# Performance work log

Measured on AMD Instinct MI355X. Metric: run time of the kernel, lower is better.

## Reference

```python
import jax, jax.numpy as jnp
import numpy as np
import math

N, L, C, H = 16, 2048, 512, 8
D = C // H  # head channels = 64


def setup_inputs() -> dict:
    key = jax.random.key(0)
    ks = jax.random.split(key, 18)
    s = 1.0 / math.sqrt(C)
    sd = 1.0 / math.sqrt(D)
    return {
        "x_q": jax.random.normal(ks[0], (N, L, C), jnp.float32),
        "x_kv": jax.random.normal(ks[1], (N, L, C), jnp.float32),
        "Wq": jax.random.normal(ks[2], (C, C), jnp.float32) * s,
        "bq": jax.random.normal(ks[3], (C,), jnp.float32) * s,
        "wqa": jax.random.normal(ks[4], (D,), jnp.float32) * sd,
        "bqa": jax.random.normal(ks[5], (1,), jnp.float32) * sd,
        "Wk": jax.random.normal(ks[6], (C, C), jnp.float32) * s,
        "bk": jax.random.normal(ks[7], (C,), jnp.float32) * s,
        "wka": jax.random.normal(ks[8], (D,), jnp.float32) * sd,
        "bka": jax.random.normal(ks[9], (1,), jnp.float32) * sd,
        "Wv": jax.random.normal(ks[10], (C, C), jnp.float32) * s,
        "bv": jax.random.normal(ks[11], (C,), jnp.float32) * s,
        "Wt": jax.random.normal(ks[12], (D, D), jnp.float32) * sd,
        "bt": jax.random.normal(ks[13], (D,), jnp.float32) * sd,
        "Wp": jax.random.normal(ks[14], (C, C), jnp.float32) * s,
        "bp": jax.random.normal(ks[15], (C,), jnp.float32) * s,
    }


def _separate_heads(x):
    # (N, L, C) -> (N, H, L, D)
    n, l, _ = x.shape
    return x.reshape(n, l, H, D).transpose(0, 2, 1, 3)


def reference(x_q, x_kv, Wq, bq, wqa, bqa, Wk, bk, wka, bka, Wv, bv, Wt, bt, Wp, bp):
    inv_sqrt_d = 1.0 / math.sqrt(D)

    # Query projection (torch Linear: y = x @ W.T + b), dropout is identity (eval)
    q = _separate_heads(x_q @ Wq.T + bq)  # (N,H,L,D)
    # Additive pooling of queries over L
    q_score = (jnp.einsum("nhld,d->nhl", q, wqa) + bqa[0]) * inv_sqrt_d
    q_weight = jax.nn.softmax(q_score, axis=-1)  # (N,H,L)
    pooled_q = jnp.einsum("nhl,nhld->nhd", q_weight, q)[:, :, None, :]  # (N,H,1,D)

    # Key projection, gated by pooled query
    k = _separate_heads(x_kv @ Wk.T + bk)  # (N,H,L,D)
    kq = k * pooled_q
    k_score = (jnp.einsum("nhld,d->nhl", kq, wka) + bka[0]) * inv_sqrt_d
    k_weight = jax.nn.softmax(k_score, axis=-1)
    pooled_k = jnp.einsum("nhl,nhld->nhd", k_weight, k)[:, :, None, :]  # (N,H,1,D)

    # Value projection, gated by pooled key, then per-head transform
    v = _separate_heads(x_kv @ Wv.T + bv)  # (N,H,L,D)
    kv = jnp.einsum("nhld,ed->nhle", v * pooled_k, Wt) + bt

    out = kv + q  # (N,H,L,D)
    out = out.transpose(0, 2, 1, 3).reshape(out.shape[0], out.shape[2], C)  # group heads
    return out @ Wp.T + bp
```

## Files before the change

kernel.cpp:

```cpp
#include <hip/hip_runtime.h>
#include <hip/hip_bf16.h>
#include <math.h>

#define NB 16
#define LL 2048
#define CC 512
#define HH 8
#define MM (NB*LL)

typedef __attribute__((ext_vector_type(8))) short bf16x8;
typedef __attribute__((ext_vector_type(4))) float f32x4;
typedef __attribute__((ext_vector_type(8))) unsigned short u16x8;

__device__ inline unsigned short f2bf(float x) {
    __hip_bfloat16 b = __float2bfloat16(x);
    return __builtin_bit_cast(unsigned short, b);
}
__device__ inline float bf2f(unsigned short u) {
    __hip_bfloat16 b = __builtin_bit_cast(__hip_bfloat16, u);
    return __bfloat162float(b);
}
__device__ inline void split2(float x, unsigned short& h, unsigned short& l) {
    unsigned short hh = f2bf(x);
    float fh = bf2f(hh);
    h = hh;
    l = f2bf(x - fh);
}

__global__ __launch_bounds__(256)
void prep_kernel(const float* __restrict__ Wq, const float* __restrict__ Wk,
                 const float* __restrict__ Wv, const float* __restrict__ Wt,
                 const float* __restrict__ bt, const float* __restrict__ Wp,
                 const float* __restrict__ bp,
                 unsigned short* __restrict__ Bqh, unsigned short* __restrict__ Bql,
                 unsigned short* __restrict__ Bkh, unsigned short* __restrict__ Bkl,
                 unsigned short* __restrict__ Bvh, unsigned short* __restrict__ Bvl,
                 unsigned short* __restrict__ WPTh, unsigned short* __restrict__ WPTl,
                 float* __restrict__ WBFP, float* __restrict__ cvec)
{
    const int t = blockIdx.x * 256 + threadIdx.x;
    const int c = t >> 10;
    const int k = t & 1023;
    unsigned short hh, ll;
    if (k < 512) {
        const int h = k >> 6, d = k & 63;
        float s = 0.f;
        #pragma unroll 8
        for (int e = 0; e < 64; ++e) s += Wt[e * 64 + d] * Wp[c * CC + h * 64 + e];
        const size_t pq = (((size_t)(k >> 3) * 512) + c) * 8 + (k & 7);
        WBFP[pq] = s;
        split2(Wq[c * CC + k], hh, ll); Bqh[pq] = hh; Bql[pq] = ll;
        split2(Wk[c * CC + k], hh, ll); Bkh[pq] = hh; Bkl[pq] = ll;
        split2(Wv[c * CC + k], hh, ll); Bvh[pq] = hh; Bvl[pq] = ll;
    } else {
        const int kl = k - 512;
        const size_t pw = (((size_t)(kl >> 3) * 512) + c) * 8 + (kl & 7);
        split2(Wp[c * CC + kl], hh, ll);
        WPTh[pw] = hh; WPTl[pw] = ll;
    }
    if (k == 0) {
        float cv = bp[c];
        for (int j = 0; j < 512; ++j) cv += bt[j & 63] * Wp[c * CC + j];
        cvec[c] = cv;
    }
}

__global__ __launch_bounds__(256)
void gate_wb(const float* __restrict__ WBFP, const float* __restrict__ pk,
             unsigned short* __restrict__ WBGh, unsigned short* __restrict__ WBGl)
{
    const int u = blockIdx.x * 256 + threadIdx.x;
    const int smp = u >> 15;
    const int r = u & 32767;
    const int kp = r >> 9, c = r & 511;
    const float* w = &WBFP[(((size_t)kp * 512) + c) * 8];
    const float* p = &pk[smp * 512 + kp * 8];
    u16x8 hv, lv;
    #pragma unroll
    for (int j = 0; j < 8; ++j) {
        unsigned short h, lo;
        split2(w[j] * p[j], h, lo);
        hv[j] = h; lv[j] = lo;
    }
    const size_t o = (((size_t)smp * 64 + kp) * 512 + c) * 8;
    *(u16x8*)&WBGh[o] = hv;
    *(u16x8*)&WBGl[o] = lv;
}

__global__ __launch_bounds__(512, 4)
void gemm_proj(const float* __restrict__ A0, const float* __restrict__ A1,
               const unsigned short* __restrict__ B0h, const unsigned short* __restrict__ B0l,
               const unsigned short* __restrict__ B1h, const unsigned short* __restrict__ B1l,
               const float* __restrict__ bias0, const float* __restrict__ bias1,
               unsigned short* __restrict__ O0h, unsigned short* __restrict__ O0l,
               unsigned short* __restrict__ O1h, unsigned short* __restrict__ O1l,
               int ntl)
{
    __shared__ __align__(16) unsigned short smem[24576];
    unsigned short* sAh = smem;
    unsigned short* sAl = smem + 4096;
    unsigned short* sBh = smem + 8192;
    unsigned short* sBl = smem + 16384;

    const int tid = threadIdx.x;
    const int flat = blockIdx.x;
    const int xcd = flat & 7, idx = flat >> 3;
    const int mt = xcd * 32 + (idx >> ntl);
    const int ntv = idx & ((1 << ntl) - 1);
    const int type = ntv >> 1;
    const int n0 = (ntv & 1) * 256;
    const int m0 = mt * 128;
    const int l = tid & 63, w = tid >> 6;
    const int wm = w >> 2, wn = w & 3;

    const float* Asrc = type ? A1 : A0;
    const unsigned short* Bh = type ? B1h : B0h;
    const unsigned short* Bl = type ? B1l : B0l;
    const float* bias = type ? bias1 : bias0;
    unsigned short* Oh = type ? O1h : O0h;
    unsigned short* Ol = type ? O1l : O0l;

    const int arow = tid & 127, akp = tid >> 7;
    const int bcol = tid & 255, bkp0 = tid >> 8;

    f32x4 acc[4][4] = {};

    float4 pa0, pa1;
    uint4 pbh0, pbh1, pbl0, pbl1;

    auto loadTile = [&](int kt) {
        const int k0 = kt * 32;
        const float* p = Asrc + (size_t)(m0 + arow) * CC + k0 + akp * 8;
        pa0 = *(const float4*)p; pa1 = *(const float4*)(p + 4);
        const int kpg = kt * 4;
        const size_t ob0 = (((size_t)(kpg + bkp0) * 512) + n0 + bcol) * 8;
        const size_t ob1 = (((size_t)(kpg + bkp0 + 2) * 512) + n0 + bcol) * 8;
        pbh0 = *(const uint4*)&Bh[ob0]; pbh1 = *(const uint4*)&Bh[ob1];
        pbl0 = *(const uint4*)&Bl[ob0]; pbl1 = *(const uint4*)&Bl[ob1];
    };

    auto storeTile = [&]() {
        float x[8];
        *(float4*)&x[0] = pa0; *(float4*)&x[4] = pa1;
        u16x8 hv, lv;
        #pragma unroll
        for (int j = 0; j < 8; ++j) { unsigned short h, lo; split2(x[j], h, lo); hv[j] = h; lv[j] = lo; }
        *(u16x8*)&sAh[(akp * 128 + arow) * 8] = hv;
        *(u16x8*)&sAl[(akp * 128 + arow) * 8] = lv;
        *(uint4*)&sBh[(bkp0 * 256 + bcol) * 8] = pbh0;
        *(uint4*)&sBh[((bkp0 + 2) * 256 + bcol) * 8] = pbh1;
        *(uint4*)&sBl[(bkp0 * 256 + bcol) * 8] = pbl0;
        *(uint4*)&sBl[((bkp0 + 2) * 256 + bcol) * 8] = pbl1;
    };

    loadTile(0);

    for (int kt = 0; kt < 16; ++kt) {
        __syncthreads();
        storeTile();
        __syncthreads();
        if (kt + 1 < 16) loadTile(kt + 1);

        const int g = l >> 4;
        const int rA = wm * 64 + (l & 15);
        const int rB = wn * 64 + (l & 15);
        const bf16x8* vAh = (const bf16x8*)sAh; const bf16x8* vAl = (const bf16x8*)sAl;
        const bf16x8* vBh = (const bf16x8*)sBh; const bf16x8* vBl = (const bf16x8*)sBl;
        bf16x8 ah[4], al[4], bh[4], bl[4];
        #pragma unroll
        for (int f = 0; f < 4; ++f) {
            ah[f] = vAh[g * 128 + rA + f * 16];
            al[f] = vAl[g * 128 + rA + f * 16];
            bh[f] = vBh[g * 256 + rB + f * 16];
            bl[f] = vBl[g * 256 + rB + f * 16];
        }
        #pragma unroll
        for (int i = 0; i < 4; ++i)
            #pragma unroll
            for (int j = 0; j < 4; ++j) {
                acc[i][j] = __builtin_amdgcn_mfma_f32_16x16x32_bf16(ah[i], bh[j], acc[i][j], 0, 0, 0);
                acc[i][j] = __builtin_amdgcn_mfma_f32_16x16x32_bf16(ah[i], bl[j], acc[i][j], 0, 0, 0);
                acc[i][j] = __builtin_amdgcn_mfma_f32_16x16x32_bf16(al[i], bh[j], acc[i][j], 0, 0, 0);
            }
    }

    const int rowb = (l >> 4) * 4, colb = l & 15;
    const int hw = wn >> 1;
    const int clbase = (wn & 1) * 64;
    unsigned short* sP = smem;
    for (int half = 0; half < 2; ++half) {
        for (int part = 0; part < 2; ++part) {
            __syncthreads();
            if (hw == half) {
                #pragma unroll
                for (int j = 0; j < 4; ++j) {
                    const float bv = bias[n0 + half * 128 + clbase + j * 16 + colb];
                    #pragma unroll
                    for (int i = 0; i < 4; ++i) {
                        #pragma unroll
                        for (int e = 0; e < 4; ++e) {
                            const int row = wm * 64 + i * 16 + rowb + e;
                            const int cl = clbase + j * 16 + colb;
                            unsigned short h, lo;
                            split2(acc[i][j][e] + bv, h, lo);
                            sP[row * 132 + cl] = part ? lo : h;
                        }
                    }
                }
            }
            __syncthreads();
            unsigned short* OP = part ? Ol : Oh;
            #pragma unroll
            for (int pass = 0; pass < 4; ++pass) {
                const int o = pass * 4 + (tid >> 7);
                const int row = tid & 127;
                const uint2 v0 = *(const uint2*)&sP[row * 132 + o * 8];
                const uint2 v1 = *(const uint2*)&sP[row * 132 + o * 8 + 4];
                const int cg = n0 + half * 128 + o * 8;
                uint4 val; val.x = v0.x; val.y = v0.y; val.z = v1.x; val.w = v1.y;
                *(uint4*)&OP[((size_t)(cg >> 3) * MM + m0 + row) * 8] = val;
            }
        }
    }
}

__global__ __launch_bounds__(512, 4)
void gemm_final(const unsigned short* __restrict__ VPh, const unsigned short* __restrict__ VPl,
                const unsigned short* __restrict__ QPh, const unsigned short* __restrict__ QPl,
                const unsigned short* __restrict__ WBGh, const unsigned short* __restrict__ WBGl,
                const unsigned short* __restrict__ WPTh, const unsigned short* __restrict__ WPTl,
                const float* __restrict__ cvec, float* __restrict__ out)
{
    __shared__ __align__(16) unsigned short smem[24576];
    unsigned short* sAh = smem;
    unsigned short* sAl = smem + 4096;
    unsigned short* sBh = smem + 8192;
    unsigned short* sBl = smem + 16384;

    const int tid = threadIdx.x;
    const int flat = blockIdx.x;
    const int xcd = flat & 7, idx = flat >> 3;
    const int mt = xcd * 32 + (idx >> 1);
    const int nt = idx & 1;
    const int n0 = nt * 256, m0 = mt * 128;
    const int l = tid & 63, w = tid >> 6;
    const int wm = w >> 2, wn = w & 3;
    const int smp = mt >> 4;

    const int arow = tid & 127, akp = tid >> 7;
    const int bcol = tid & 255, bkp0 = tid >> 8;

    f32x4 acc[4][4] = {};

    uint4 pah, pal, pbh0, pbh1, pbl0, pbl1;

    auto loadTile = [&](int kt) {
        const int ktl = kt & 15;
        const unsigned short* Ah_ = (kt < 16) ? VPh : QPh;
        const unsigned short* Al_ = (kt < 16) ? VPl : QPl;
        const size_t ao = (((size_t)ktl * 4 + akp) * MM + m0 + arow) * 8;
        pah = *(const uint4*)&Ah_[ao];
        pal = *(const uint4*)&Al_[ao];
        const unsigned short* Bh_;
        const unsigned short* Bl_;
        size_t bb;
        if (kt < 16) { Bh_ = WBGh + (size_t)smp * 262144; Bl_ = WBGl + (size_t)smp * 262144; bb = kt * 4; }
        else         { Bh_ = WPTh; Bl_ = WPTl; bb = (kt - 16) * 4; }
        const size_t ob0 = ((bb + bkp0) * 512 + n0 + bcol) * 8;
        const size_t ob1 = ((bb + bkp0 + 2) * 512 + n0 + bcol) * 8;
        pbh0 = *(const uint4*)&Bh_[ob0]; pbh1 = *(const uint4*)&Bh_[ob1];
        pbl0 = *(const uint4*)&Bl_[ob0]; pbl1 = *(const uint4*)&Bl_[ob1];
    };

    auto storeTile = [&]() {
        *(uint4*)&sAh[(akp * 128 + arow) * 8] = pah;
        *(uint4*)&sAl[(akp * 128 + arow) * 8] = pal;
        *(uint4*)&sBh[(bkp0 * 256 + bcol) * 8] = pbh0;
        *(uint4*)&sBh[((bkp0 + 2) * 256 + bcol) * 8] = pbh1;
        *(uint4*)&sBl[(bkp0 * 256 + bcol) * 8] = pbl0;
        *(uint4*)&sBl[((bkp0 + 2) * 256 + bcol) * 8] = pbl1;
    };

    loadTile(0);

    for (int kt = 0; kt < 32; ++kt) {
        __syncthreads();
        storeTile();
        __syncthreads();
        if (kt + 1 < 32) loadTile(kt + 1);

        const int g = l >> 4;
        const int rA = wm * 64 + (l & 15);
        const int rB = wn * 64 + (l & 15);
        const bf16x8* vAh = (const bf16x8*)sAh; const bf16x8* vAl = (const bf16x8*)sAl;
        const bf16x8* vBh = (const bf16x8*)sBh; const bf16x8* vBl = (const bf16x8*)sBl;
        bf16x8 ah[4], al[4], bh[4], bl[4];
        #pragma unroll
        for (int f = 0; f < 4; ++f) {
            ah[f] = vAh[g * 128 + rA + f * 16];
            al[f] = vAl[g * 128 + rA + f * 16];
            bh[f] = vBh[g * 256 + rB + f * 16];
            bl[f] = vBl[g * 256 + rB + f * 16];
        }
        #pragma unroll
        for (int i = 0; i < 4; ++i)
            #pragma unroll
            for (int j = 0; j < 4; ++j) {
                acc[i][j] = __builtin_amdgcn_mfma_f32_16x16x32_bf16(ah[i], bh[j], acc[i][j], 0, 0, 0);
                acc[i][j] = __builtin_amdgcn_mfma_f32_16x16x32_bf16(ah[i], bl[j], acc[i][j], 0, 0, 0);
                acc[i][j] = __builtin_amdgcn_mfma_f32_16x16x32_bf16(al[i], bh[j], acc[i][j], 0, 0, 0);
            }
    }

    const int rowb = (l >> 4) * 4, colb = l & 15;
    #pragma unroll
    for (int j = 0; j < 4; ++j) {
        const int c = n0 + wn * 64 + j * 16 + colb;
        const float bv = cvec[c];
        #pragma unroll
        for (int i = 0; i < 4; ++i) {
            const int r = m0 + wm * 64 + i * 16 + rowb;
            #pragma unroll
            for (int e = 0; e < 4; ++e)
                out[(size_t)(r + e) * CC + c] = acc[i][j][e] + bv;
        }
    }
}

__global__ __launch_bounds__(256)
void pool_stage1(const unsigned short* __restrict__ Ph, const unsigned short* __restrict__ Pl,
                 const float* __restrict__ wvec, const float* __restrict__ bscal,
                 float* __restrict__ partials, int modeK)
{
    __shared__ float sm[256];
    __shared__ float se[4];
    const int nh = blockIdx.x, chunk = blockIdx.y;
    const int n = nh >> 3, h = nh & 7;
    const int tid = threadIdx.x;
    const int wave = tid >> 6, d = tid & 63;
    const float wv = modeK ? wvec[nh * 64 + d] : wvec[d];
    const float b = bscal[0];
    const size_t rbase = ((size_t)(h * 8 + (d >> 3))) * MM + (size_t)n * LL;
    const int kc = d & 7;
    float accv = 0.f, acce = 0.f;
    const int l0 = chunk * 128 + wave;
    #pragma unroll 4
    for (int it = 0; it < 32; ++it) {
        const int ll = l0 + it * 4;
        const size_t a = (rbase + ll) * 8 + kc;
        const float x = bf2f(Ph[a]) + bf2f(Pl[a]);
        float s = x * wv;
        s += __shfl_xor(s, 1, 64);
        s += __shfl_xor(s, 2, 64);
        s += __shfl_xor(s, 4, 64);
        s += __shfl_xor(s, 8, 64);
        s += __shfl_xor(s, 16, 64);
        s += __shfl_xor(s, 32, 64);
        const float e = expf((s + b) * 0.125f);
        accv += e * x;
        acce += e;
    }
    sm[tid] = accv;
    if (d == 0) se[wave] = acce;
    __syncthreads();
    if (wave == 0) {
        const float pv = sm[d] + sm[64 + d] + sm[128 + d] + sm[192 + d];
        float* pr = partials + ((size_t)nh * 16 + chunk) * 65;
        pr[d] = pv;
        if (d == 0) pr[64] = se[0] + se[1] + se[2] + se[3];
    }
}

__global__ __launch_bounds__(64)
void pool_stage2(const float* __restrict__ partials, const float* __restrict__ postmul,
                 float* __restrict__ pooled)
{
    const int nh = blockIdx.x, d = threadIdx.x;
    float pv = 0.f, pe = 0.f;
    #pragma unroll
    for (int c = 0; c < 16; ++c) {
        const float* pr = partials + ((size_t)nh * 16 + c) * 65;
        pv += pr[d];
        pe += pr[64];
    }
    float p = pv / pe;
    if (postmul) p *= postmul[d];
    pooled[nh * 64 + d] = p;
}

#define OFF_BQH   0ull
#define OFF_BQL   524288ull
#define OFF_BKH   1048576ull
#define OFF_BKL   1572864ull
#define OFF_BVH   2097152ull
#define OFF_BVL   2621440ull
#define OFF_WPTH  3145728ull
#define OFF_WPTL  3670016ull
#define OFF_WBFP  4194304ull
#define OFF_CVEC  5242880ull
#define OFF_GQ    5246976ull
#define OFF_PK    5279744ull
#define OFF_PART  5312512ull
#define OFF_WBGH  6291456ull
#define OFF_WBGL  14680064ull
#define OFF_QPH   23068672ull
#define OFF_QPL   56623104ull
#define OFF_KPH   90177536ull
#define OFF_KPL   123731968ull

extern "C" void kernel_launch(void* const* d_in, const int* in_sizes, int n_in,
                              void* d_out, int out_size, void* d_ws, size_t ws_size,
                              hipStream_t stream) {
    const float* x_q  = (const float*)d_in[0];
    const float* x_kv = (const float*)d_in[1];
    const float* Wq   = (const float*)d_in[2];
    const float* bq   = (const float*)d_in[3];
    const float* wqa  = (const float*)d_in[4];
    const float* bqa  = (const float*)d_in[5];
    const float* Wk   = (const float*)d_in[6];
    const float* bk   = (const float*)d_in[7];
    const float* wka  = (const float*)d_in[8];
    const float* bka  = (const float*)d_in[9];
    const float* Wv   = (const float*)d_in[10];
    const float* bv   = (const float*)d_in[11];
    const float* Wt   = (const float*)d_in[12];
    const float* bt   = (const float*)d_in[13];
    const float* Wp   = (const float*)d_in[14];
    const float* bp   = (const float*)d_in[15];
    float* out = (float*)d_out;
    char* ws = (char*)d_ws;

    unsigned short* Bqh  = (unsigned short*)(ws + OFF_BQH);
    unsigned short* Bql  = (unsigned short*)(ws + OFF_BQL);
    unsigned short* Bkh  = (unsigned short*)(ws + OFF_BKH);
    unsigned short* Bkl  = (unsigned short*)(ws + OFF_BKL);
    unsigned short* Bvh  = (unsigned short*)(ws + OFF_BVH);
    unsigned short* Bvl  = (unsigned short*)(ws + OFF_BVL);
    unsigned short* WPTh = (unsigned short*)(ws + OFF_WPTH);
    unsigned short* WPTl = (unsigned short*)(ws + OFF_WPTL);
    float* WBFP = (float*)(ws + OFF_WBFP);
    float* cvec = (float*)(ws + OFF_CVEC);
    float* gq   = (float*)(ws + OFF_GQ);
    float* pk   = (float*)(ws + OFF_PK);
    float* part = (float*)(ws + OFF_PART);
    unsigned short* WBGh = (unsigned short*)(ws + OFF_WBGH);
    unsigned short* WBGl = (unsigned short*)(ws + OFF_WBGL);
    unsigned short* QPh  = (unsigned short*)(ws + OFF_QPH);
    unsigned short* QPl  = (unsigned short*)(ws + OFF_QPL);
    unsigned short* KPh  = (unsigned short*)(ws + OFF_KPH);
    unsigned short* KPl  = (unsigned short*)(ws + OFF_KPL);

    const dim3 pgrid(NB * HH, 16);

    prep_kernel<<<2048, 256, 0, stream>>>(Wq, Wk, Wv, Wt, bt, Wp, bp,
                                          Bqh, Bql, Bkh, Bkl, Bvh, Bvl,
                                          WPTh, WPTl, WBFP, cvec);
    gemm_proj<<<1024, 512, 0, stream>>>(x_q, x_kv, Bqh, Bql, Bkh, Bkl, bq, bk,
                                        QPh, QPl, KPh, KPl, 2);
    pool_stage1<<<pgrid, 256, 0, stream>>>(QPh, QPl, wqa, bqa, part, 0);
    pool_stage2<<<NB * HH, 64, 0, stream>>>(part, wka, gq);
    pool_stage1<<<pgrid, 256, 0, stream>>>(KPh, KPl, gq, bka, part, 1);
    pool_stage2<<<NB * HH, 64, 0, stream>>>(part, nullptr, pk);
    gate_wb<<<2048, 256, 0, stream>>>(WBFP, pk, WBGh, WBGl);
    gemm_proj<<<512, 512, 0, stream>>>(x_kv, x_kv, Bvh, Bvl, Bvh, Bvl, bv, bv,
                                       KPh, KPl, KPh, KPl, 1);
    gemm_final<<<512, 512, 0, stream>>>(KPh, KPl, QPh, QPl, WBGh, WBGl,
                                        WPTh, WPTl, cvec, out);
}
```

Baseline: 487.4 us.

## Pool queries and keys directly from inputs, skipping the full K projection

Folds the additive-pooling score vectors into the projection weights (Uq = Wq^T wqa, Uk = Wk^T gated wka), so the softmax scores and pooled sums are computed directly on raw x_q/x_kv. Pooled vectors are then projected once per batch item, which removes the full K projection GEMM and its bf16 hi/lo intermediate. The Q and V projections now share one GEMM launch. In exchange it adds a register-heavy pooling pass that reads x twice, a serial per-batch combine kernel, and a change in numerical rounding order.

```diff
diff --git a/kernel.cpp b/kernel.cpp
--- a/kernel.cpp
+++ b/kernel.cpp
@@ -28,12 +28,10 @@
 }
 
 __global__ __launch_bounds__(256)
-void prep_kernel(const float* __restrict__ Wq, const float* __restrict__ Wk,
-                 const float* __restrict__ Wv, const float* __restrict__ Wt,
-                 const float* __restrict__ bt, const float* __restrict__ Wp,
-                 const float* __restrict__ bp,
+void prep_kernel(const float* __restrict__ Wq, const float* __restrict__ Wv,
+                 const float* __restrict__ Wt, const float* __restrict__ bt,
+                 const float* __restrict__ Wp, const float* __restrict__ bp,
                  unsigned short* __restrict__ Bqh, unsigned short* __restrict__ Bql,
-                 unsigned short* __restrict__ Bkh, unsigned short* __restrict__ Bkl,
                  unsigned short* __restrict__ Bvh, unsigned short* __restrict__ Bvl,
                  unsigned short* __restrict__ WPTh, unsigned short* __restrict__ WPTl,
                  float* __restrict__ WBFP, float* __restrict__ cvec)
@@ -50,7 +48,6 @@
         const size_t pq = (((size_t)(k >> 3) * 512) + c) * 8 + (k & 7);
         WBFP[pq] = s;
         split2(Wq[c * CC + k], hh, ll); Bqh[pq] = hh; Bql[pq] = ll;
-        split2(Wk[c * CC + k], hh, ll); Bkh[pq] = hh; Bkl[pq] = ll;
         split2(Wv[c * CC + k], hh, ll); Bvh[pq] = hh; Bvl[pq] = ll;
     } else {
         const int kl = k - 512;
@@ -62,6 +59,153 @@
         float cv = bp[c];
         for (int j = 0; j < 512; ++j) cv += bt[j & 63] * Wp[c * CC + j];
         cvec[c] = cv;
+    }
+}
+
+__global__ __launch_bounds__(512)
+void uq_kernel(const float* __restrict__ Wq, const float* __restrict__ wqa,
+               const float* __restrict__ bqa, const float* __restrict__ bq,
+               float* __restrict__ Uq, float* __restrict__ qc)
+{
+    const int c = threadIdx.x;
+    float u[8] = {0.f,0.f,0.f,0.f,0.f,0.f,0.f,0.f};
+    for (int d = 0; d < 64; ++d) {
+        const float wv = wqa[d];
+        #pragma unroll
+        for (int h = 0; h < 8; ++h) u[h] += Wq[((size_t)(h * 64 + d)) * 512 + c] * wv;
+    }
+    #pragma unroll
+    for (int h = 0; h < 8; ++h) Uq[c * 8 + h] = u[h];
+    if (c < 8) {
+        float s = 0.f;
+        for (int d = 0; d < 64; ++d) s += bq[c * 64 + d] * wqa[d];
+        qc[c] = s + bqa[0];
+    }
+}
+
+__global__ __launch_bounds__(256)
+void pool_pass1(const float* __restrict__ x, const float* __restrict__ U, int ustride,
+                const float* __restrict__ cst, int cstride, float* __restrict__ part)
+{
+    __shared__ float ps2[2][8][512];
+    __shared__ float pe[4][8];
+    const int n = blockIdx.x, ch = blockIdx.y;
+    const int tid = threadIdx.x, wave = tid >> 6, lane = tid & 63;
+    const int c8 = lane * 8;
+    float u[64];
+    {
+        const float* Ub = U + (size_t)n * ustride + c8 * 8;
+        #pragma unroll
+        for (int j = 0; j < 16; ++j) *(float4*)&u[j * 4] = *(const float4*)&Ub[j * 4];
+    }
+    float cl[8];
+    #pragma unroll
+    for (int h = 0; h < 8; ++h) cl[h] = cst[n * cstride + h];
+    float acc[64];
+    #pragma unroll
+    for (int j = 0; j < 64; ++j) acc[j] = 0.f;
+    float ae[8] = {0.f,0.f,0.f,0.f,0.f,0.f,0.f,0.f};
+    const int l0 = ch * 64 + wave * 16;
+    const float* xb = x + ((size_t)n * LL + l0) * CC + c8;
+    for (int it = 0; it < 16; ++it) {
+        float xs[8];
+        *(float4*)&xs[0] = *(const float4*)&xb[(size_t)it * CC];
+        *(float4*)&xs[4] = *(const float4*)&xb[(size_t)it * CC + 4];
+        #pragma unroll
+        for (int h = 0; h < 8; ++h) {
+            float s = xs[0]*u[h]    + xs[1]*u[8+h]  + xs[2]*u[16+h] + xs[3]*u[24+h]
+                    + xs[4]*u[32+h] + xs[5]*u[40+h] + xs[6]*u[48+h] + xs[7]*u[56+h];
+            s += __shfl_xor(s, 1, 64);  s += __shfl_xor(s, 2, 64);
+            s += __shfl_xor(s, 4, 64);  s += __shfl_xor(s, 8, 64);
+            s += __shfl_xor(s, 16, 64); s += __shfl_xor(s, 32, 64);
+            const float e = __expf((s + cl[h]) * 0.125f);
+            ae[h] += e;
+            #pragma unroll
+            for (int j = 0; j < 8; ++j) acc[h * 8 + j] += e * xs[j];
+        }
+    }
+    if (wave < 2) {
+        #pragma unroll
+        for (int h = 0; h < 8; ++h)
+            #pragma unroll
+            for (int j = 0; j < 8; ++j) ps2[wave][h][c8 + j] = acc[h * 8 + j];
+    }
+    if (lane == 0) {
+        #pragma unroll
+        for (int h = 0; h < 8; ++h) pe[wave][h] = ae[h];
+    }
+    __syncthreads();
+    if (wave >= 2) {
+        #pragma unroll
+        for (int h = 0; h < 8; ++h)
+            #pragma unroll
+            for (int j = 0; j < 8; ++j) ps2[wave - 2][h][c8 + j] += acc[h * 8 + j];
+    }
+    __syncthreads();
+    float* pb = part + ((size_t)(n * 32 + ch)) * 4104;
+    for (int q = tid; q < 4096; q += 256) {
+        const int h = q >> 9, c = q & 511;
+        pb[q] = ps2[0][h][c] + ps2[1][h][c];
+    }
+    if (tid < 8) pb[4096 + tid] = pe[0][tid] + pe[1][tid] + pe[2][tid] + pe[3][tid];
+}
+
+__global__ __launch_bounds__(512)
+void pool_combine(const float* __restrict__ part,
+                  const float* __restrict__ W1, const float* __restrict__ b1,
+                  const float* __restrict__ wka,
+                  const float* __restrict__ Wk, const float* __restrict__ bk,
+                  const float* __restrict__ bka,
+                  float* __restrict__ gq, float* __restrict__ Uk,
+                  float* __restrict__ kc, float* __restrict__ pk, int mode)
+{
+    __shared__ float px[8][512];
+    __shared__ float inv[8];
+    __shared__ float gql[8][64];
+    const int n = blockIdx.x;
+    const int tid = threadIdx.x;
+    const float* pbase = part + (size_t)n * 32 * 4104;
+    for (int q = tid; q < 4096; q += 512) {
+        float s = 0.f;
+        for (int c2 = 0; c2 < 32; ++c2) s += pbase[(size_t)c2 * 4104 + q];
+        px[q >> 9][q & 511] = s;
+    }
+    if (tid < 8) {
+        float s = 0.f;
+        for (int c2 = 0; c2 < 32; ++c2) s += pbase[(size_t)c2 * 4104 + 4096 + tid];
+        inv[tid] = 1.f / s;
+    }
+    __syncthreads();
+    const int h = tid >> 6, d = tid & 63;
+    const int row = h * 64 + d;
+    float s = 0.f;
+    const float* wr = W1 + (size_t)row * 512;
+    #pragma unroll 8
+    for (int c = 0; c < 512; ++c) s += px[h][c] * wr[c];
+    const float pooled = s * inv[h] + b1[row];
+    if (mode == 0) {
+        const float g = pooled * wka[d];
+        gq[n * 512 + row] = g;
+        gql[h][d] = g;
+        __syncthreads();
+        const int c = tid & 511;
+        float uk[8];
+        #pragma unroll
+        for (int hh = 0; hh < 8; ++hh) uk[hh] = 0.f;
+        for (int dd = 0; dd < 64; ++dd) {
+            #pragma unroll
+            for (int hh = 0; hh < 8; ++hh)
+                uk[hh] += Wk[((size_t)(hh * 64 + dd)) * 512 + c] * gql[hh][dd];
+        }
+        #pragma unroll
+        for (int hh = 0; hh < 8; ++hh) Uk[(size_t)n * 4096 + c * 8 + hh] = uk[hh];
+        if (tid < 8) {
+            float kcv = 0.f;
+            for (int dd = 0; dd < 64; ++dd) kcv += bk[tid * 64 + dd] * gql[tid][dd];
+            kc[n * 8 + tid] = kcv + bka[0];
+        }
+    } else {
+        pk[n * 512 + row] = pooled;
     }
 }
 
@@ -327,86 +471,27 @@
     }
 }
 
-__global__ __launch_bounds__(256)
-void pool_stage1(const unsigned short* __restrict__ Ph, const unsigned short* __restrict__ Pl,
-                 const float* __restrict__ wvec, const float* __restrict__ bscal,
-                 float* __restrict__ partials, int modeK)
-{
-    __shared__ float sm[256];
-    __shared__ float se[4];
-    const int nh = blockIdx.x, chunk = blockIdx.y;
-    const int n = nh >> 3, h = nh & 7;
-    const int tid = threadIdx.x;
-    const int wave = tid >> 6, d = tid & 63;
-    const float wv = modeK ? wvec[nh * 64 + d] : wvec[d];
-    const float b = bscal[0];
-    const size_t rbase = ((size_t)(h * 8 + (d >> 3))) * MM + (size_t)n * LL;
-    const int kc = d & 7;
-    float accv = 0.f, acce = 0.f;
-    const int l0 = chunk * 128 + wave;
-    #pragma unroll 4
-    for (int it = 0; it < 32; ++it) {
-        const int ll = l0 + it * 4;
-        const size_t a = (rbase + ll) * 8 + kc;
-        const float x = bf2f(Ph[a]) + bf2f(Pl[a]);
-        float s = x * wv;
-        s += __shfl_xor(s, 1, 64);
-        s += __shfl_xor(s, 2, 64);
-        s += __shfl_xor(s, 4, 64);
-        s += __shfl_xor(s, 8, 64);
-        s += __shfl_xor(s, 16, 64);
-        s += __shfl_xor(s, 32, 64);
-        const float e = expf((s + b) * 0.125f);
-        accv += e * x;
-        acce += e;
-    }
-    sm[tid] = accv;
-    if (d == 0) se[wave] = acce;
-    __syncthreads();
-    if (wave == 0) {
-        const float pv = sm[d] + sm[64 + d] + sm[128 + d] + sm[192 + d];
-        float* pr = partials + ((size_t)nh * 16 + chunk) * 65;
-        pr[d] = pv;
-        if (d == 0) pr[64] = se[0] + se[1] + se[2] + se[3];
-    }
-}
-
-__global__ __launch_bounds__(64)
-void pool_stage2(const float* __restrict__ partials, const float* __restrict__ postmul,
-                 float* __restrict__ pooled)
-{
-    const int nh = blockIdx.x, d = threadIdx.x;
-    float pv = 0.f, pe = 0.f;
-    #pragma unroll
-    for (int c = 0; c < 16; ++c) {
-        const float* pr = partials + ((size_t)nh * 16 + c) * 65;
-        pv += pr[d];
-        pe += pr[64];
-    }
-    float p = pv / pe;
-    if (postmul) p *= postmul[d];
-    pooled[nh * 64 + d] = p;
-}
-
 #define OFF_BQH   0ull
 #define OFF_BQL   524288ull
-#define OFF_BKH   1048576ull
-#define OFF_BKL   1572864ull
-#define OFF_BVH   2097152ull
-#define OFF_BVL   2621440ull
-#define OFF_WPTH  3145728ull
-#define OFF_WPTL  3670016ull
-#define OFF_WBFP  4194304ull
-#define OFF_CVEC  5242880ull
-#define OFF_GQ    5246976ull
-#define OFF_PK    5279744ull
-#define OFF_PART  5312512ull
-#define OFF_WBGH  6291456ull
-#define OFF_WBGL  14680064ull
-#define OFF_QPH   23068672ull
-#define OFF_QPL   56623104ull
-#define OFF_KPH   90177536ull
-#define OFF_KPL   123731968ull
+#define OFF_BVH   1048576ull
+#define OFF_BVL   1572864ull
+#define OFF_WPTH  2097152ull
+#define OFF_WPTL  2621440ull
+#define OFF_WBFP  3145728ull
+#define OFF_CVEC  4194304ull
+#define OFF_UQ    4198400ull
+#define OFF_QC    4214784ull
+#define OFF_UK    4215040ull
+#define OFF_KC    4477184ull
+#define OFF_GQ    4477952ull
+#define OFF_PK    4510720ull
+#define OFF_PART  4543488ull
+#define OFF_WBGH  13107200ull
+#define OFF_WBGL  21495808ull
+#define OFF_QPH   29884416ull
+#define OFF_QPL   63438848ull
+#define OFF_VPH   96993280ull
+#define OFF_VPL   130547712ull
 
 extern "C" void kernel_launch(void* const* d_in, const int* in_sizes, int n_in,
                               void* d_out, int out_size, void* d_ws, size_t ws_size,
@@ -432,14 +517,16 @@
 
     unsigned short* Bqh  = (unsigned short*)(ws + OFF_BQH);
     unsigned short* Bql  = (unsigned short*)(ws + OFF_BQL);
-    unsigned short* Bkh  = (unsigned short*)(ws + OFF_BKH);
-    unsigned short* Bkl  = (unsigned short*)(ws + OFF_BKL);
     unsigned short* Bvh  = (unsigned short*)(ws + OFF_BVH);
     unsigned short* Bvl  = (unsigned short*)(ws + OFF_BVL);
     unsigned short* WPTh = (unsigned short*)(ws + OFF_WPTH);
     unsigned short* WPTl = (unsigned short*)(ws + OFF_WPTL);
     float* WBFP = (float*)(ws + OFF_WBFP);
     float* cvec = (float*)(ws + OFF_CVEC);
+    float* Uq   = (float*)(ws + OFF_UQ);
+    float* qc   = (float*)(ws + OFF_QC);
+    float* Uk   = (float*)(ws + OFF_UK);
+    float* kc   = (float*)(ws + OFF_KC);
     float* gq   = (float*)(ws + OFF_GQ);
     float* pk   = (float*)(ws + OFF_PK);
     float* part = (float*)(ws + OFF_PART);
@@ -447,23 +534,23 @@
     unsigned short* WBGl = (unsigned short*)(ws + OFF_WBGL);
     unsigned short* QPh  = (unsigned short*)(ws + OFF_QPH);
     unsigned short* QPl  = (unsigned short*)(ws + OFF_QPL);
-    unsigned short* KPh  = (unsigned short*)(ws + OFF_KPH);
-    unsigned short* KPl  = (unsigned short*)(ws + OFF_KPL);
-
-    const dim3 pgrid(NB * HH, 16);
-
-    prep_kernel<<<2048, 256, 0, stream>>>(Wq, Wk, Wv, Wt, bt, Wp, bp,
-                                          Bqh, Bql, Bkh, Bkl, Bvh, Bvl,
-                                          WPTh, WPTl, WBFP, cvec);
-    gemm_proj<<<1024, 512, 0, stream>>>(x_q, x_kv, Bqh, Bql, Bkh, Bkl, bq, bk,
-                                        QPh, QPl, KPh, KPl, 2);
-    pool_stage1<<<pgrid, 256, 0, stream>>>(QPh, QPl, wqa, bqa, part, 0);
-    pool_stage2<<<NB * HH, 64, 0, stream>>>(part, wka, gq);
-    pool_stage1<<<pgrid, 256, 0, stream>>>(KPh, KPl, gq, bka, part, 1);
-    pool_stage2<<<NB * HH, 64, 0, stream>>>(part, nullptr, pk);
+    unsigned short* VPh  = (unsigned short*)(ws + OFF_VPH);
+    unsigned short* VPl  = (unsigned short*)(ws + OFF_VPL);
+
+    const dim3 pgrid(NB, 32);
+
+    prep_kernel<<<2048, 256, 0, stream>>>(Wq, Wv, Wt, bt, Wp, bp,
+                                          Bqh, Bql, Bvh, Bvl, WPTh, WPTl, WBFP, cvec);
+    uq_kernel<<<1, 512, 0, stream>>>(Wq, wqa, bqa, bq, Uq, qc);
+    pool_pass1<<<pgrid, 256, 0, stream>>>(x_q, Uq, 0, qc, 0, part);
+    pool_combine<<<NB, 512, 0, stream>>>(part, Wq, bq, wka, Wk, bk, bka,
+                                         gq, Uk, kc, nullptr, 0);
+    pool_pass1<<<pgrid, 256, 0, stream>>>(x_kv, Uk, 4096, kc, 8, part);
+    pool_combine<<<NB, 512, 0, stream>>>(part, Wk, bk, nullptr, nullptr, nullptr, nullptr,
+                                         nullptr, nullptr, nullptr, pk, 1);
     gate_wb<<<2048, 256, 0, stream>>>(WBFP, pk, WBGh, WBGl);
-    gemm_proj<<<512, 512, 0, stream>>>(x_kv, x_kv, Bvh, Bvl, Bvh, Bvl, bv, bv,
-                                       KPh, KPl, KPh, KPl, 1);
-    gemm_final<<<512, 512, 0, stream>>>(KPh, KPl, QPh, QPl, WBGh, WBGl,
+    gemm_proj<<<1024, 512, 0, stream>>>(x_q, x_kv, Bqh, Bql, Bvh, Bvl, bq, bv,
+                                        QPh, QPl, VPh, VPl, 2);
+    gemm_final<<<512, 512, 0, stream>>>(VPh, VPl, QPh, QPl, WBGh, WBGl,
                                         WPTh, WPTl, cvec, out);
 }
```

New measurement: 564.8 us. +15.9%, slower.
